# Performance work log

Hardware: AMD Instinct MI355X
Metric: run time of the kernel (lower is better)

Reference implementation:

```python
import jax, jax.numpy as jnp
import numpy as np

B, LQ, C = 4, 4096, 384
NH, NL, NP = 6, 1, 4
HL, WL = 64, 64
LV = HL * WL
DH = C // NH
EPS = 1e-6


def layer_norm(x, g, b):
    mu = jnp.mean(x, axis=-1, keepdims=True)
    var = jnp.mean(jnp.square(x - mu), axis=-1, keepdims=True)
    return (x - mu) * jax.lax.rsqrt(var + EPS) * g + b


def ms_deform_attn_core(value, spatial_shapes, level_start_index, loc, attn_w):
    # value [B,LV,NH,DH]; loc [B,LQ,NH,NL,NP,2] in [0,1]; attn_w [B,LQ,NH,NL,NP]
    ss = np.asarray(spatial_shapes)
    lsi = np.asarray(level_start_index)
    Bv, _, nH, dh = value.shape
    Lq = loc.shape[1]
    nP = loc.shape[4]
    out = jnp.zeros((Bv, Lq, nH, dh), value.dtype)
    for l in range(loc.shape[3]):
        Hl, Wl = int(ss[l, 0]), int(ss[l, 1])
        st = int(lsi[l])
        vflat = value[:, st:st + Hl * Wl]  # [B, Hl*Wl, nH, dh]
        xy = loc[:, :, :, l]               # [B,LQ,nH,NP,2]
        # grid_sample(align_corners=False): pixel = loc * size - 0.5
        x = xy[..., 0] * Wl - 0.5
        y = xy[..., 1] * Hl - 0.5
        x0 = jnp.floor(x)
        y0 = jnp.floor(y)
        wx = x - x0
        wy = y - y0
        x0i = x0.astype(jnp.int32)
        y0i = y0.astype(jnp.int32)

        def gather(xi, yi):
            # zero padding outside the feature map (padding_mode='zeros')
            valid = (xi >= 0) & (xi < Wl) & (yi >= 0) & (yi < Hl)
            idx = jnp.clip(yi, 0, Hl - 1) * Wl + jnp.clip(xi, 0, Wl - 1)  # [B,LQ,nH,NP]
            idx2 = idx.transpose(0, 1, 3, 2).reshape(Bv, Lq * nP, nH)
            g = jnp.take_along_axis(vflat, idx2[..., None], axis=1)       # [B,LQ*NP,nH,dh]
            g = g.reshape(Bv, Lq, nP, nH, dh).transpose(0, 1, 3, 2, 4)    # [B,LQ,nH,NP,dh]
            return g * valid[..., None].astype(value.dtype)

        samp = (gather(x0i, y0i) * ((1 - wx) * (1 - wy))[..., None]
                + gather(x0i + 1, y0i) * (wx * (1 - wy))[..., None]
                + gather(x0i, y0i + 1) * ((1 - wx) * wy)[..., None]
                + gather(x0i + 1, y0i + 1) * (wx * wy)[..., None])
        out = out + jnp.einsum('bqhpd,bqhp->bqhd', samp, attn_w[:, :, :, l])
    return out.reshape(Bv, Lq, nH * dh)


def setup_inputs() -> dict:
    key = jax.random.key(0)
    ks = jax.random.split(key, 12)
    s = 0.02
    return {
        'query': jax.random.normal(ks[0], (B, LQ, C), jnp.float32),
        'reference_points': jax.random.uniform(ks[1], (B, LQ, NL, 2), dtype=jnp.float32),
        'feat': jax.random.normal(ks[2], (B, LV, C), jnp.float32),
        'spatial_shapes': jnp.array([[HL, WL]], jnp.int32),
        'level_start_index': jnp.array([0], jnp.int32),
        'ln_q_g': jnp.ones((C,), jnp.float32), 'ln_q_b': jnp.zeros((C,), jnp.float32),
        'ln_f_g': jnp.ones((C,), jnp.float32), 'ln_f_b': jnp.zeros((C,), jnp.float32),
        'gamma': jax.random.normal(ks[3], (C,), jnp.float32) * 0.1,
        'Wv': jax.random.normal(ks[4], (C, C), jnp.float32) * s,
        'bv': jnp.zeros((C,), jnp.float32),
        'Wo': jax.random.normal(ks[5], (C, NH * NL * NP * 2), jnp.float32) * s,
        'bo': jax.random.normal(ks[6], (NH * NL * NP * 2,), jnp.float32) * 0.5,
        'Wa': jax.random.normal(ks[7], (C, NH * NL * NP), jnp.float32) * s,
        'ba': jnp.zeros((NH * NL * NP,), jnp.float32),
        'Wout': jax.random.normal(ks[8], (C, C), jnp.float32) * s,
        'bout': jnp.zeros((C,), jnp.float32),
    }


def reference(query, reference_points, feat, spatial_shapes, level_start_index,
              ln_q_g, ln_q_b, ln_f_g, ln_f_b, gamma,
              Wv, bv, Wo, bo, Wa, ba, Wout, bout):
    q = layer_norm(query, ln_q_g, ln_q_b)
    f = layer_norm(feat, ln_f_g, ln_f_b)
    value = (f @ Wv + bv).reshape(B, LV, NH, DH)
    offsets = (q @ Wo + bo).reshape(B, LQ, NH, NL, NP, 2)
    attn_w = jax.nn.softmax((q @ Wa + ba).reshape(B, LQ, NH, NL * NP), axis=-1)
    attn_w = attn_w.reshape(B, LQ, NH, NL, NP)
    # offset normalizer is (W, H) per level
    norm = jnp.stack([spatial_shapes[:, 1], spatial_shapes[:, 0]], -1).astype(jnp.float32)
    loc = reference_points[:, :, None, :, None, :] + offsets / norm[None, None, None, :, None, :]
    attn = ms_deform_attn_core(value, spatial_shapes, level_start_index, loc, attn_w)
    attn = attn @ Wout + bout
    return query + gamma * attn
```

## Files before the change

kernel.cpp:

```cpp
#include <hip/hip_runtime.h>
#include <math.h>

#define B_    4
#define LQ_   4096
#define C_    384
#define NH_   6
#define NP_   4
#define HL_   64
#define WL_   64
#define LV_   (HL_ * WL_)
#define ROWS_ (B_ * LQ_)
#define EPS_  1e-6f
#define NOFF_ 48
#define NLOG_ 24

typedef unsigned short u16;
typedef __bf16 bf16x8 __attribute__((ext_vector_type(8)));
typedef float  f32x4  __attribute__((ext_vector_type(4)));

__device__ __forceinline__ float bf2f(u16 v) {
    unsigned int u = ((unsigned int)v) << 16;
    return __uint_as_float(u);
}
__device__ __forceinline__ u16 f2bf(float f) {
    unsigned int u = __float_as_uint(f);
    u += 0x7fff + ((u >> 16) & 1);
    return (u16)(u >> 16);
}

__device__ __forceinline__ f32x4 mfma16(bf16x8 a, bf16x8 b, f32x4 c) {
    return __builtin_amdgcn_mfma_f32_16x16x32_bf16(a, b, c, 0, 0, 0);
}

__device__ __forceinline__ void gl_lds16(const u16* g, u16* l) {
    __builtin_amdgcn_global_load_lds(
        (const __attribute__((address_space(1))) unsigned int*)g,
        (__attribute__((address_space(3))) unsigned int*)l, 16, 0, 0);
}

#define LN_BLOCKS_   8192
#define PREP_BLOCKS_ 1273

__global__ __launch_bounds__(256) void ln_prep(
    const float* __restrict__ query, const float* __restrict__ feat,
    const float* __restrict__ qg, const float* __restrict__ qbv,
    const float* __restrict__ fg, const float* __restrict__ fbv,
    u16* __restrict__ qout, u16* __restrict__ fout,
    const float* __restrict__ Wv, const float* __restrict__ Wout,
    const float* __restrict__ Wo, const float* __restrict__ Wa,
    const float* __restrict__ bo, const float* __restrict__ ba,
    u16* __restrict__ WvT, u16* __restrict__ WoutT, u16* __restrict__ WcT,
    float* __restrict__ bias_c)
{
    if (blockIdx.x < LN_BLOCKS_) {
        int wid  = threadIdx.x >> 6;
        int lane = threadIdx.x & 63;
        int row  = blockIdx.x * 4 + wid;
        const float *src, *g, *bsh;
        u16* dst;
        int r;
        if (row < ROWS_) { src = query; g = qg; bsh = qbv; dst = qout; r = row; }
        else             { src = feat;  g = fg; bsh = fbv; dst = fout; r = row - ROWS_; }

        const float* x = src + (size_t)r * C_;
        float v[6];
        float s = 0.f;
#pragma unroll
        for (int k = 0; k < 6; ++k) { v[k] = x[lane + 64 * k]; s += v[k]; }
#pragma unroll
        for (int off = 32; off; off >>= 1) s += __shfl_xor(s, off);
        float mu = s * (1.f / C_);

        float s2 = 0.f;
#pragma unroll
        for (int k = 0; k < 6; ++k) { float d = v[k] - mu; s2 += d * d; }
#pragma unroll
        for (int off = 32; off; off >>= 1) s2 += __shfl_xor(s2, off);
        float rs = rsqrtf(s2 * (1.f / C_) + EPS_);

        u16* y = dst + (size_t)r * C_;
#pragma unroll
        for (int k = 0; k < 6; ++k) {
            int c = lane + 64 * k;
            y[c] = f2bf((v[k] - mu) * rs * g[c] + bsh[c]);
        }
    } else {
        const int KN = 384 * 384;
        int idx = (blockIdx.x - LN_BLOCKS_) * 256 + threadIdx.x;
        if (idx < KN) {
            int n = idx / 384, k = idx - n * 384;
            WvT[idx] = f2bf(Wv[k * 384 + n]);
        } else if (idx < 2 * KN) {
            int t = idx - KN;
            int n = t / 384, k = t - n * 384;
            WoutT[t] = f2bf(Wout[k * 384 + n]);
        } else if (idx < 2 * KN + 80 * 384) {
            int t = idx - 2 * KN;
            int n = t / 384, k = t - n * 384;
            float v = (n < 48) ? Wo[k * 48 + n] : (n < 72 ? Wa[k * 24 + (n - 48)] : 0.f);
            WcT[t] = f2bf(v);
        } else if (idx < 2 * KN + 80 * 384 + 80) {
            int n = idx - (2 * KN + 80 * 384);
            bias_c[n] = (n < 48) ? bo[n] : (n < 72 ? ba[n - 48] : 0.f);
        }
    }
}

__global__ __launch_bounds__(256) void gemm_combined(
    const u16* __restrict__ fb, const u16* __restrict__ qb,
    const u16* __restrict__ WvT, const u16* __restrict__ WcT,
    const float* __restrict__ bv, const float* __restrict__ bias_c,
    u16* __restrict__ valb, float* __restrict__ offs, float* __restrict__ logits)
{
    const int K = 384;
    __shared__ __align__(16) u16 As[128 * 32];
    __shared__ __align__(16) u16 Bs[80 * 32];

    int g    = blockIdx.x;
    int tid  = threadIdx.x;
    int lane = tid & 63, wid = tid >> 6;
    int fr = lane & 15, quad = lane >> 4;

    int srow = tid >> 2;
    int scol = (tid & 3) * 8;

    if (g < 768) {
        int m0 = (g / 6) * 128, n0 = (g % 6) * 64;
        const u16* agp0 = fb  + (size_t)(m0 + srow) * K + scol;
        const u16* agp1 = fb  + (size_t)(m0 + 64 + srow) * K + scol;
        const u16* bgp  = WvT + (size_t)(n0 + srow) * K + scol;
        u16* al0 = As + tid * 8;  u16* al1 = As + 2048 + tid * 8;
        u16* bl  = Bs + tid * 8;

        int wm = (wid >> 1) * 64, wn = (wid & 1) * 32;

        f32x4 zero = {0.f, 0.f, 0.f, 0.f};
        f32x4 acc[4][2];
#pragma unroll
        for (int i = 0; i < 4; ++i)
#pragma unroll
            for (int j = 0; j < 2; ++j) acc[i][j] = zero;

        for (int k0 = 0; k0 < K; k0 += 32) {
            gl_lds16(agp0 + k0, al0);
            gl_lds16(agp1 + k0, al1);
            gl_lds16(bgp  + k0, bl);
            __syncthreads();
            bf16x8 af[4], bfr[2];
#pragma unroll
            for (int i = 0; i < 4; ++i)
                af[i] = *(bf16x8*)&As[(wm + i * 16 + fr) * 32 + quad * 8];
#pragma unroll
            for (int j = 0; j < 2; ++j)
                bfr[j] = *(bf16x8*)&Bs[(wn + j * 16 + fr) * 32 + quad * 8];
#pragma unroll
            for (int i = 0; i < 4; ++i)
#pragma unroll
                for (int j = 0; j < 2; ++j)
                    acc[i][j] = mfma16(af[i], bfr[j], acc[i][j]);
            __syncthreads();
        }

#pragma unroll
        for (int i = 0; i < 4; ++i) {
            int row = m0 + wm + i * 16 + quad * 4;
#pragma unroll
            for (int j = 0; j < 2; ++j) {
                int col = n0 + wn + j * 16 + fr;
                float bcol = bv[col];
#pragma unroll
                for (int r = 0; r < 4; ++r)
                    valb[(size_t)(row + r) * C_ + col] = f2bf(acc[i][j][r] + bcol);
            }
        }
    } else {
        int m0 = (g - 768) * 128;
        const u16* agp0 = qb + (size_t)(m0 + srow) * K + scol;
        const u16* agp1 = qb + (size_t)(m0 + 64 + srow) * K + scol;
        u16* al0 = As + tid * 8;  u16* al1 = As + 2048 + tid * 8;
        const u16* bgp0 = WcT + (size_t)srow * K + scol;
        const u16* bgp1 = WcT + (size_t)(64 + srow) * K + scol;
        u16* bl0 = Bs + tid * 8;
        u16* bl1 = Bs + 2048 + tid * 8;

        int wm = wid * 32;

        f32x4 zero = {0.f, 0.f, 0.f, 0.f};
        f32x4 acc[2][5];
#pragma unroll
        for (int i = 0; i < 2; ++i)
#pragma unroll
            for (int j = 0; j < 5; ++j) acc[i][j] = zero;

        for (int k0 = 0; k0 < K; k0 += 32) {
            gl_lds16(agp0 + k0, al0);
            gl_lds16(agp1 + k0, al1);
            gl_lds16(bgp0 + k0, bl0);
            if (tid < 64) gl_lds16(bgp1 + k0, bl1);
            __syncthreads();
            bf16x8 af[2], bfr[5];
#pragma unroll
            for (int i = 0; i < 2; ++i)
                af[i] = *(bf16x8*)&As[(wm + i * 16 + fr) * 32 + quad * 8];
#pragma unroll
            for (int j = 0; j < 5; ++j)
                bfr[j] = *(bf16x8*)&Bs[(j * 16 + fr) * 32 + quad * 8];
#pragma unroll
            for (int i = 0; i < 2; ++i)
#pragma unroll
                for (int j = 0; j < 5; ++j)
                    acc[i][j] = mfma16(af[i], bfr[j], acc[i][j]);
            __syncthreads();
        }

#pragma unroll
        for (int i = 0; i < 2; ++i) {
            int row = m0 + wm + i * 16 + quad * 4;
#pragma unroll
            for (int j = 0; j < 5; ++j) {
                int col = j * 16 + fr;
                if (col < 72) {
                    float bcol = bias_c[col];
#pragma unroll
                    for (int r = 0; r < 4; ++r) {
                        float v = acc[i][j][r] + bcol;
                        if (col < 48) offs[(size_t)(row + r) * NOFF_ + col] = v;
                        else          logits[(size_t)(row + r) * NLOG_ + (col - 48)] = v;
                    }
                }
            }
        }
    }
}

#define QT_   16
#define APAD_ 392

__global__ __launch_bounds__(512) void fused_sample_out(
    const u16*  __restrict__ value,
    const float* __restrict__ rp,
    const float* __restrict__ offs,
    const float* __restrict__ logits,
    const u16*  __restrict__ WoutT,
    const float* __restrict__ bout,
    const float* __restrict__ gamma,
    const float* __restrict__ query,
    float* __restrict__ out)
{
    __shared__ float meta[QT_ * NH_ * NP_ * 4];
    __shared__ __align__(16) u16 attn_s[QT_ * APAD_];

    int t = threadIdx.x;
    int g = blockIdx.x;
    int b     = (g & 7) >> 1;
    int local = ((g >> 3) << 1) | (g & 1);
    int m0 = b * LQ_ + local * QT_;

    if (t < QT_ * NH_ * NP_) {
        int q = t / (NH_ * NP_);
        int rem = t - q * (NH_ * NP_);
        int h = rem >> 2, p = rem & 3;
        int r = m0 + q;

        const float* lg = logits + (size_t)r * NLOG_ + h * 4;
        float l0 = lg[0], l1 = lg[1], l2 = lg[2], l3 = lg[3];
        float mx = fmaxf(fmaxf(l0, l1), fmaxf(l2, l3));
        float e0 = expf(l0 - mx), e1 = expf(l1 - mx);
        float e2 = expf(l2 - mx), e3 = expf(l3 - mx);
        float den = e0 + e1 + e2 + e3;
        float ep = (p == 0) ? e0 : (p == 1) ? e1 : (p == 2) ? e2 : e3;
        float aw = ep / den;

        float rx = rp[(size_t)r * 2 + 0];
        float ry = rp[(size_t)r * 2 + 1];
        float ox = offs[(size_t)r * NOFF_ + (h * 4 + p) * 2 + 0];
        float oy = offs[(size_t)r * NOFF_ + (h * 4 + p) * 2 + 1];
        float x = rx * (float)WL_ + ox - 0.5f;
        float y = ry * (float)HL_ + oy - 0.5f;
        float x0f = floorf(x), y0f = floorf(y);
        int x0 = (int)x0f, y0 = (int)y0f;

        int midx = t * 4;
        meta[midx + 0] = x - x0f;
        meta[midx + 1] = y - y0f;
        meta[midx + 2] = aw;
        meta[midx + 3] = __int_as_float((y0 << 16) | (x0 & 0xffff));
    }
    __syncthreads();

#pragma unroll
    for (int j = 0; j < 2; ++j) {
        int v = t + 512 * j;
        if (v < QT_ * 48) {
            int q = v / 48, dc = v - q * 48;
            int h = dc >> 3;
            int col0 = dc << 3;
            const u16* vbase = value + (size_t)b * LV_ * C_ + col0;

            float acc[8] = {0.f, 0.f, 0.f, 0.f, 0.f, 0.f, 0.f, 0.f};
#pragma unroll
            for (int p = 0; p < NP_; ++p) {
                int midx = ((q * NH_ + h) * NP_ + p) * 4;
                float wx = meta[midx + 0];
                float wy = meta[midx + 1];
                float aw = meta[midx + 2];
                int packed = __float_as_int(meta[midx + 3]);
                int x0 = (packed << 16) >> 16;
                int y0 = packed >> 16;
#pragma unroll
                for (int c = 0; c < 4; ++c) {
                    int xi = x0 + (c & 1);
                    int yi = y0 + (c >> 1);
                    bool valid = (xi >= 0) && (xi < WL_) && (yi >= 0) && (yi < HL_);
                    int xc = xi < 0 ? 0 : (xi > WL_ - 1 ? WL_ - 1 : xi);
                    int yc = yi < 0 ? 0 : (yi > HL_ - 1 ? HL_ - 1 : yi);
                    float w = ((c & 1) ? wx : 1.f - wx) * ((c >> 1) ? wy : 1.f - wy) * aw;
                    w = valid ? w : 0.f;
                    bf16x8 vv = *(const bf16x8*)(vbase + (size_t)(yc * WL_ + xc) * C_);
#pragma unroll
                    for (int e = 0; e < 8; ++e) acc[e] += w * (float)vv[e];
                }
            }
            u16* dst = attn_s + q * APAD_ + col0;
#pragma unroll
            for (int e = 0; e < 8; ++e) dst[e] = f2bf(acc[e]);
        }
    }
    __syncthreads();

    int lane = t & 63, wid = t >> 6;
    int fr = lane & 15, quad = lane >> 4;
    int wn0 = wid * 48;

    f32x4 zero = {0.f, 0.f, 0.f, 0.f};
    f32x4 acc[3];
#pragma unroll
    for (int j = 0; j < 3; ++j) acc[j] = zero;

    for (int k0 = 0; k0 < 384; k0 += 32) {
        bf16x8 a0 = *(bf16x8*)&attn_s[fr * APAD_ + k0 + quad * 8];
#pragma unroll
        for (int nt = 0; nt < 3; ++nt) {
            bf16x8 bb = *(const bf16x8*)(WoutT + (size_t)(wn0 + nt * 16 + fr) * 384 + k0 + quad * 8);
            acc[nt] = mfma16(a0, bb, acc[nt]);
        }
    }

#pragma unroll
    for (int nt = 0; nt < 3; ++nt) {
        int col = wn0 + nt * 16 + fr;
        float gm = gamma[col], bc = bout[col];
#pragma unroll
        for (int rr = 0; rr < 4; ++rr) {
            size_t o = (size_t)(m0 + quad * 4 + rr) * C_ + col;
            out[o] = query[o] + gm * (acc[nt][rr] + bc);
        }
    }
}

extern "C" void kernel_launch(void* const* d_in, const int* in_sizes, int n_in,
                              void* d_out, int out_size, void* d_ws, size_t ws_size,
                              hipStream_t stream)
{
    const float* query  = (const float*)d_in[0];
    const float* rp     = (const float*)d_in[1];
    const float* feat   = (const float*)d_in[2];
    const float* gamma  = (const float*)d_in[9];
    const float* Wv     = (const float*)d_in[10];
    const float* bv     = (const float*)d_in[11];
    const float* Wo     = (const float*)d_in[12];
    const float* bo     = (const float*)d_in[13];
    const float* Wa     = (const float*)d_in[14];
    const float* ba     = (const float*)d_in[15];
    const float* Wout   = (const float*)d_in[16];
    const float* bout   = (const float*)d_in[17];
    float* out = (float*)d_out;

    u16* wsu    = (u16*)d_ws;
    u16* qb     = wsu;
    u16* fb     = qb    + (size_t)ROWS_ * C_;
    u16* valb   = fb    + (size_t)ROWS_ * C_;
    u16* WvT    = valb  + (size_t)ROWS_ * C_;
    u16* WoutT  = WvT   + 384 * 384;
    u16* WcT    = WoutT + 384 * 384;
    float* offs   = (float*)(WcT + 80 * 384);
    float* logits = offs + (size_t)ROWS_ * NOFF_;
    float* bias_c = logits + (size_t)ROWS_ * NLOG_;

    ln_prep<<<LN_BLOCKS_ + PREP_BLOCKS_, 256, 0, stream>>>(
        query, feat,
        (const float*)d_in[5], (const float*)d_in[6],
        (const float*)d_in[7], (const float*)d_in[8],
        qb, fb, Wv, Wout, Wo, Wa, bo, ba, WvT, WoutT, WcT, bias_c);

    gemm_combined<<<896, 256, 0, stream>>>(fb, qb, WvT, WcT, bv, bias_c,
                                           valb, offs, logits);

    fused_sample_out<<<ROWS_ / QT_, 512, 0, stream>>>(
        valb, rp, offs, logits, WoutT, bout, gamma, query, out);
}
```

Measured before the change: 191.5 us.

## Enlarge value GEMM tiles and compute sampling metadata per thread without LDS

The value-projection GEMM now uses 128x128 tiles instead of 128x64, which halves its block count (896 to 512 total) and doubles the MMA work per wave to get more reuse of each loaded A tile. The sampling kernel drops the shared-memory metadata stage and its barrier. Each thread instead loads logits, offsets and reference points with vector loads and recomputes softmax and bilinear coordinates itself, using fast __expf. In exchange, the redundant per-thread math and the extra accumulator registers could lower occupancy, and 512 blocks may underfill the GPU.

```diff
diff --git a/kernel.cpp b/kernel.cpp
--- a/kernel.cpp
+++ b/kernel.cpp
@@ -114,7 +114,7 @@
 {
     const int K = 384;
     __shared__ __align__(16) u16 As[128 * 32];
-    __shared__ __align__(16) u16 Bs[80 * 32];
+    __shared__ __align__(16) u16 Bs[128 * 32];
 
     int g    = blockIdx.x;
     int tid  = threadIdx.x;
@@ -124,39 +124,41 @@
     int srow = tid >> 2;
     int scol = (tid & 3) * 8;
 
-    if (g < 768) {
-        int m0 = (g / 6) * 128, n0 = (g % 6) * 64;
+    if (g < 384) {
+        int m0 = (g / 3) * 128, n0 = (g % 3) * 128;
         const u16* agp0 = fb  + (size_t)(m0 + srow) * K + scol;
         const u16* agp1 = fb  + (size_t)(m0 + 64 + srow) * K + scol;
-        const u16* bgp  = WvT + (size_t)(n0 + srow) * K + scol;
+        const u16* bgp0 = WvT + (size_t)(n0 + srow) * K + scol;
+        const u16* bgp1 = WvT + (size_t)(n0 + 64 + srow) * K + scol;
         u16* al0 = As + tid * 8;  u16* al1 = As + 2048 + tid * 8;
-        u16* bl  = Bs + tid * 8;
-
-        int wm = (wid >> 1) * 64, wn = (wid & 1) * 32;
+        u16* bl0 = Bs + tid * 8;  u16* bl1 = Bs + 2048 + tid * 8;
+
+        int wm = (wid >> 1) * 64, wn = (wid & 1) * 64;
 
         f32x4 zero = {0.f, 0.f, 0.f, 0.f};
-        f32x4 acc[4][2];
+        f32x4 acc[4][4];
 #pragma unroll
         for (int i = 0; i < 4; ++i)
 #pragma unroll
-            for (int j = 0; j < 2; ++j) acc[i][j] = zero;
+            for (int j = 0; j < 4; ++j) acc[i][j] = zero;
 
         for (int k0 = 0; k0 < K; k0 += 32) {
             gl_lds16(agp0 + k0, al0);
             gl_lds16(agp1 + k0, al1);
-            gl_lds16(bgp  + k0, bl);
+            gl_lds16(bgp0 + k0, bl0);
+            gl_lds16(bgp1 + k0, bl1);
             __syncthreads();
-            bf16x8 af[4], bfr[2];
+            bf16x8 af[4], bfr[4];
 #pragma unroll
             for (int i = 0; i < 4; ++i)
                 af[i] = *(bf16x8*)&As[(wm + i * 16 + fr) * 32 + quad * 8];
 #pragma unroll
-            for (int j = 0; j < 2; ++j)
+            for (int j = 0; j < 4; ++j)
                 bfr[j] = *(bf16x8*)&Bs[(wn + j * 16 + fr) * 32 + quad * 8];
 #pragma unroll
             for (int i = 0; i < 4; ++i)
 #pragma unroll
-                for (int j = 0; j < 2; ++j)
+                for (int j = 0; j < 4; ++j)
                     acc[i][j] = mfma16(af[i], bfr[j], acc[i][j]);
             __syncthreads();
         }
@@ -165,7 +167,7 @@
         for (int i = 0; i < 4; ++i) {
             int row = m0 + wm + i * 16 + quad * 4;
 #pragma unroll
-            for (int j = 0; j < 2; ++j) {
+            for (int j = 0; j < 4; ++j) {
                 int col = n0 + wn + j * 16 + fr;
                 float bcol = bv[col];
 #pragma unroll
@@ -174,7 +176,7 @@
             }
         }
     } else {
-        int m0 = (g - 768) * 128;
+        int m0 = (g - 384) * 128;
         const u16* agp0 = qb + (size_t)(m0 + srow) * K + scol;
         const u16* agp1 = qb + (size_t)(m0 + 64 + srow) * K + scol;
         u16* al0 = As + tid * 8;  u16* al1 = As + 2048 + tid * 8;
@@ -247,7 +249,6 @@
     const float* __restrict__ query,
     float* __restrict__ out)
 {
-    __shared__ float meta[QT_ * NH_ * NP_ * 4];
     __shared__ __align__(16) u16 attn_s[QT_ * APAD_];
 
     int t = threadIdx.x;
@@ -256,37 +257,7 @@
     int local = ((g >> 3) << 1) | (g & 1);
     int m0 = b * LQ_ + local * QT_;
 
-    if (t < QT_ * NH_ * NP_) {
-        int q = t / (NH_ * NP_);
-        int rem = t - q * (NH_ * NP_);
-        int h = rem >> 2, p = rem & 3;
-        int r = m0 + q;
-
-        const float* lg = logits + (size_t)r * NLOG_ + h * 4;
-        float l0 = lg[0], l1 = lg[1], l2 = lg[2], l3 = lg[3];
-        float mx = fmaxf(fmaxf(l0, l1), fmaxf(l2, l3));
-        float e0 = expf(l0 - mx), e1 = expf(l1 - mx);
-        float e2 = expf(l2 - mx), e3 = expf(l3 - mx);
-        float den = e0 + e1 + e2 + e3;
-        float ep = (p == 0) ? e0 : (p == 1) ? e1 : (p == 2) ? e2 : e3;
-        float aw = ep / den;
-
-        float rx = rp[(size_t)r * 2 + 0];
-        float ry = rp[(size_t)r * 2 + 1];
-        float ox = offs[(size_t)r * NOFF_ + (h * 4 + p) * 2 + 0];
-        float oy = offs[(size_t)r * NOFF_ + (h * 4 + p) * 2 + 1];
-        float x = rx * (float)WL_ + ox - 0.5f;
-        float y = ry * (float)HL_ + oy - 0.5f;
-        float x0f = floorf(x), y0f = floorf(y);
-        int x0 = (int)x0f, y0 = (int)y0f;
-
-        int midx = t * 4;
-        meta[midx + 0] = x - x0f;
-        meta[midx + 1] = y - y0f;
-        meta[midx + 2] = aw;
-        meta[midx + 3] = __int_as_float((y0 << 16) | (x0 & 0xffff));
-    }
-    __syncthreads();
+    const u16* vbatch = value + (size_t)b * LV_ * C_;
 
 #pragma unroll
     for (int j = 0; j < 2; ++j) {
@@ -295,18 +266,30 @@
             int q = v / 48, dc = v - q * 48;
             int h = dc >> 3;
             int col0 = dc << 3;
-            const u16* vbase = value + (size_t)b * LV_ * C_ + col0;
-
+            int r = m0 + q;
+
+            float4 lg  = *(const float4*)(logits + (size_t)r * NLOG_ + h * 4);
+            float2 rpv = *(const float2*)(rp + (size_t)r * 2);
+            float4 of0 = *(const float4*)(offs + (size_t)r * NOFF_ + h * 8);
+            float4 of1 = *(const float4*)(offs + (size_t)r * NOFF_ + h * 8 + 4);
+
+            float mx = fmaxf(fmaxf(lg.x, lg.y), fmaxf(lg.z, lg.w));
+            float e0 = __expf(lg.x - mx), e1 = __expf(lg.y - mx);
+            float e2 = __expf(lg.z - mx), e3 = __expf(lg.w - mx);
+            float rden = 1.f / (e0 + e1 + e2 + e3);
+            float aws[4] = {e0 * rden, e1 * rden, e2 * rden, e3 * rden};
+            float oxs[4] = {of0.x, of0.z, of1.x, of1.z};
+            float oys[4] = {of0.y, of0.w, of1.y, of1.w};
+
+            const u16* vbase = vbatch + col0;
             float acc[8] = {0.f, 0.f, 0.f, 0.f, 0.f, 0.f, 0.f, 0.f};
 #pragma unroll
             for (int p = 0; p < NP_; ++p) {
-                int midx = ((q * NH_ + h) * NP_ + p) * 4;
-                float wx = meta[midx + 0];
-                float wy = meta[midx + 1];
-                float aw = meta[midx + 2];
-                int packed = __float_as_int(meta[midx + 3]);
-                int x0 = (packed << 16) >> 16;
-                int y0 = packed >> 16;
+                float x = rpv.x * (float)WL_ + oxs[p] - 0.5f;
+                float y = rpv.y * (float)HL_ + oys[p] - 0.5f;
+                float x0f = floorf(x), y0f = floorf(y);
+                float wx = x - x0f, wy = y - y0f;
+                int x0 = (int)x0f, y0 = (int)y0f;
 #pragma unroll
                 for (int c = 0; c < 4; ++c) {
                     int xi = x0 + (c & 1);
@@ -314,7 +297,7 @@
                     bool valid = (xi >= 0) && (xi < WL_) && (yi >= 0) && (yi < HL_);
                     int xc = xi < 0 ? 0 : (xi > WL_ - 1 ? WL_ - 1 : xi);
                     int yc = yi < 0 ? 0 : (yi > HL_ - 1 ? HL_ - 1 : yi);
-                    float w = ((c & 1) ? wx : 1.f - wx) * ((c >> 1) ? wy : 1.f - wy) * aw;
+                    float w = ((c & 1) ? wx : 1.f - wx) * ((c >> 1) ? wy : 1.f - wy) * aws[p];
                     w = valid ? w : 0.f;
                     bf16x8 vv = *(const bf16x8*)(vbase + (size_t)(yc * WL_ + xc) * C_);
 #pragma unroll
@@ -393,7 +376,7 @@
         (const float*)d_in[7], (const float*)d_in[8],
         qb, fb, Wv, Wout, Wo, Wa, bo, ba, WvT, WoutT, WcT, bias_c);
 
-    gemm_combined<<<896, 256, 0, stream>>>(fb, qb, WvT, WcT, bv, bias_c,
+    gemm_combined<<<512, 256, 0, stream>>>(fb, qb, WvT, WcT, bv, bias_c,
                                            valb, offs, logits);
 
     fused_sample_out<<<ROWS_ / QT_, 512, 0, stream>>>(
```

After: 186.3 us. -2.7%, faster.
